# Kernel optimization log

Hardware: AMD Instinct MI355X
Metric: run time of the kernel (lower is better)

Reference implementation:

```python
import jax, jax.numpy as jnp
import numpy as np

EPS = 1e-8


def setup_inputs() -> dict:
    key = jax.random.key(0)
    k1, k2, k3 = jax.random.split(key, 3)
    B, N, M, C = 4, 4096, 16384, 256
    xyz = jax.random.normal(k1, (B * N, 3), dtype=jnp.float32)
    new_xyz = jax.random.normal(k2, (B * M, 3), dtype=jnp.float32)
    feat = jax.random.normal(k3, (B * N, C), dtype=jnp.float32)
    offset = jnp.arange(1, B + 1, dtype=jnp.int64) * N      # [4096, 8192, 12288, 16384]
    new_offset = jnp.arange(1, B + 1, dtype=jnp.int64) * M  # [16384, ..., 65536]
    return {"xyz": xyz, "new_xyz": new_xyz, "feat": feat,
            "offset": offset, "new_offset": new_offset, "k": 3}


def _interpolate(xyz_b, new_xyz_b, feat_b, k):
    # xyz_b: [B,N,3], new_xyz_b: [B,M,3], feat_b: [B,N,C]
    # pairwise squared distances via GEMM: [B,M,N]
    q2 = jnp.sum(new_xyz_b * new_xyz_b, axis=-1, keepdims=True)        # [B,M,1]
    s2 = jnp.sum(xyz_b * xyz_b, axis=-1)[:, None, :]                   # [B,1,N]
    cross = jnp.einsum('bmd,bnd->bmn', new_xyz_b, xyz_b)               # [B,M,N]
    d2 = q2 + s2 - 2.0 * cross                                         # [B,M,N]
    neg_d2, idx = jax.lax.top_k(-d2, k)                                # [B,M,k]
    dist = jnp.sqrt(jnp.maximum(-neg_d2, 1e-12))                       # euclidean, like knnquery
    dist_recip = 1.0 / (dist + EPS)
    weight = dist_recip / jnp.sum(dist_recip, axis=-1, keepdims=True)  # [B,M,k]
    gathered = jax.vmap(lambda f, i: f[i])(feat_b, idx)                # [B,M,k,C]
    return jnp.einsum('bmkc,bmk->bmc', gathered, weight)               # [B,M,C]


def reference(xyz, new_xyz, feat, offset, new_offset, k):
    B = offset.shape[0]
    N = xyz.shape[0] // B
    M = new_xyz.shape[0] // B
    C = feat.shape[1]
    # uniform offsets -> reshape into per-cloud batches
    out = _interpolate(xyz.reshape(B, N, 3), new_xyz.reshape(B, M, 3),
                       feat.reshape(B, N, C), k)
    return out.reshape(B * M, C)
```

## Files before the change

kernel.cpp:

```cpp
#include <hip/hip_runtime.h>
#include <float.h>


#define QPL   2
#define QPB   128
#define SPLIT 8
#define KEY_INIT 0x7FEFFFFFFFFFFFFFULL

#define NCA   16
#define NC    (NCA * NCA * NCA)
#define GMIN  (-4.0f)
#define HCELL (0.5f)
#define INVH  (2.0f)
#define SLACK (1e-3f)

typedef float v2f __attribute__((ext_vector_type(2)));

__device__ __forceinline__ double mk_key(float d2, int j) {
    unsigned long long u =
        ((unsigned long long)(unsigned)__float_as_uint(d2) << 32) | (unsigned)j;
    return __longlong_as_double(u);
}

__device__ __forceinline__ void ins3(double key, double& k0, double& k1,
                                     double& k2) {
    const double n0 = fmin(key, k0);
    const double n1 = fmin(fmax(key, k0), k1);
    const double n2 = fmin(fmax(key, k1), k2);
    k0 = n0; k1 = n1; k2 = n2;
}

__device__ __forceinline__ v2f dist2_pair(const v2f qx2, const v2f qy2,
                                          const v2f qz2, const v2f q22,
                                          const float4 p) {
    #pragma clang fp contract(off)
    const v2f px = {p.x, p.x};
    const v2f py = {p.y, p.y};
    const v2f pz = {p.z, p.z};
    const v2f pw = {p.w, p.w};
    const v2f t0 = qx2 * px;
    const v2f t1 = qy2 * py;
    const v2f t2 = t0 + t1;
    const v2f t3 = qz2 * pz;
    const v2f cr = t2 + t3;
    const v2f qs = q22 + pw;
    const v2f cc = cr + cr;
    const v2f d2 = qs - cc;
    return d2;
}

__device__ __forceinline__ float dist2_scalar(float qx, float qy, float qz,
                                              float q2, const float4 p) {
    #pragma clang fp contract(off)
    const float t0 = qx * p.x;
    const float t1 = qy * p.y;
    const float t2 = t0 + t1;
    const float t3 = qz * p.z;
    const float cr = t2 + t3;
    const float qs = q2 + p.w;
    const float cc = cr + cr;
    const float d2 = qs - cc;
    return d2;
}

__device__ __forceinline__ float sum_sq3(float x, float y, float z) {
    return __fadd_rn(__fadd_rn(__fmul_rn(x, x), __fmul_rn(y, y)),
                     __fmul_rn(z, z));
}

__device__ __forceinline__ int clampi(int v, int lo, int hi) {
    return v < lo ? lo : (v > hi ? hi : v);
}

__device__ __forceinline__ void cell3(float x, float y, float z,
                                      int& cx, int& cy, int& cz) {
    cx = clampi((int)floorf((x - GMIN) * INVH), 0, NCA - 1);
    cy = clampi((int)floorf((y - GMIN) * INVH), 0, NCA - 1);
    cz = clampi((int)floorf((z - GMIN) * INVH), 0, NCA - 1);
}

__global__ void grid_histo(const float* __restrict__ xyz,
                           const float* __restrict__ new_xyz,
                           int* __restrict__ cnt, int* __restrict__ qcnt,
                           int N, int M, int B) {
    const int i = blockIdx.x * blockDim.x + threadIdx.x;
    const int totalP = B * N;
    if (i < totalP) {
        const int b = i / N;
        int cx, cy, cz;
        cell3(xyz[(size_t)i * 3 + 0], xyz[(size_t)i * 3 + 1],
              xyz[(size_t)i * 3 + 2], cx, cy, cz);
        atomicAdd(&cnt[b * NC + (cz * NCA + cy) * NCA + cx], 1);
    } else {
        const int qi = i - totalP;
        if (qi < B * M) {
            const int b = qi / M;
            int cx, cy, cz;
            cell3(new_xyz[(size_t)qi * 3 + 0], new_xyz[(size_t)qi * 3 + 1],
                  new_xyz[(size_t)qi * 3 + 2], cx, cy, cz);
            atomicAdd(&qcnt[b * NC + (cz * NCA + cy) * NCA + cx], 1);
        }
    }
}

__global__ __launch_bounds__(256) void grid_scan(
    const int* __restrict__ cnt, int* __restrict__ start,
    const int* __restrict__ qcnt, int* __restrict__ qstart,
    int N, int M, int B) {
    const int blk = blockIdx.x;
    const bool isQ = blk >= B;
    const int b = isQ ? blk - B : blk;
    const int* __restrict__ src = isQ ? qcnt : cnt;
    int* __restrict__ dst = isQ ? qstart : start;
    const int base = isQ ? b * M : b * N;
    const int t = threadIdx.x;
    const int CH = NC / 256;

    int s = 0;
    for (int j = 0; j < CH; ++j) s += src[b * NC + t * CH + j];

    __shared__ int parts[256];
    parts[t] = s;
    __syncthreads();
    for (int off = 1; off < 256; off <<= 1) {
        int v = 0;
        if (t >= off) v = parts[t - off];
        __syncthreads();
        parts[t] += v;
        __syncthreads();
    }
    int run = base + (t == 0 ? 0 : parts[t - 1]);
    for (int j = 0; j < CH; ++j) {
        dst[b * NC + t * CH + j] = run;
        run += src[b * NC + t * CH + j];
    }
    if (!isQ && b == B - 1 && t == 255) dst[B * NC] = B * N;
}

__global__ void grid_scatter(const float* __restrict__ xyz,
                             const float* __restrict__ new_xyz,
                             int* __restrict__ cnt, int* __restrict__ qcnt,
                             const int* __restrict__ start,
                             const int* __restrict__ qstart,
                             float4* __restrict__ spts, int* __restrict__ sidx,
                             int* __restrict__ qsrt,
                             int N, int M, int B) {
    const int i = blockIdx.x * blockDim.x + threadIdx.x;
    const int totalP = B * N;
    if (i < totalP) {
        const int b = i / N;
        const float sx = xyz[(size_t)i * 3 + 0];
        const float sy = xyz[(size_t)i * 3 + 1];
        const float sz = xyz[(size_t)i * 3 + 2];
        int cx, cy, cz;
        cell3(sx, sy, sz, cx, cy, cz);
        const int g = b * NC + (cz * NCA + cy) * NCA + cx;
        const int slot = start[g] + (atomicSub(&cnt[g], 1) - 1);
        spts[slot] = make_float4(sx, sy, sz, sum_sq3(sx, sy, sz));
        sidx[slot] = i - b * N;
    } else {
        const int qi = i - totalP;
        if (qi < B * M) {
            const int b = qi / M;
            int cx, cy, cz;
            cell3(new_xyz[(size_t)qi * 3 + 0], new_xyz[(size_t)qi * 3 + 1],
                  new_xyz[(size_t)qi * 3 + 2], cx, cy, cz);
            const int g = b * NC + (cz * NCA + cy) * NCA + cx;
            const int slot = qstart[g] + (atomicSub(&qcnt[g], 1) - 1);
            qsrt[slot] = qi;
        }
    }
}

__global__ __launch_bounds__(256, 8) void fp_knn_gather(
    const float* __restrict__ new_xyz,
    const float4* __restrict__ spts, const int* __restrict__ sidx,
    const int* __restrict__ start, const int* __restrict__ qsrt,
    const float4* __restrict__ feat4, float4* __restrict__ out4,
    int N, int M, int B) {
    __shared__ int   s_jb[16][3];
    __shared__ float s_wb[16][3];
    __shared__ int   s_qid[16];

    const int tid = threadIdx.x;
    const int grp = tid >> 4;
    const int s   = tid & 15;
    const int p   = blockIdx.x * 16 + grp;
    const int qid = qsrt[p];
    const int b   = qid / M;
    const int bNC = b * NC;

    const float qx = new_xyz[(size_t)qid * 3 + 0];
    const float qy = new_xyz[(size_t)qid * 3 + 1];
    const float qz = new_xyz[(size_t)qid * 3 + 2];
    const float q2 = sum_sq3(qx, qy, qz);

    int cx, cy, cz;
    cell3(qx, qy, qz, cx, cy, cz);

    const float bx0 = GMIN + (float)cx * HCELL;
    const float by0 = GMIN + (float)cy * HCELL;
    const float bz0 = GMIN + (float)cz * HCELL;
    const float ex = fmaxf(fmaxf(bx0 - qx, qx - (bx0 + HCELL)), 0.0f);
    const float ey = fmaxf(fmaxf(by0 - qy, qy - (by0 + HCELL)), 0.0f);
    const float ez = fmaxf(fmaxf(bz0 - qz, qz - (bz0 + HCELL)), 0.0f);
    const float e = fmaxf(ex, fmaxf(ey, ez));

    double k0 = __longlong_as_double(KEY_INIT), k1 = k0, k2 = k0;

    auto seg = [&](int x0, int x1, int cy2, int cz2) {
        const int rowbase = bNC + (cz2 * NCA + cy2) * NCA;
        const int j0 = start[rowbase + x0];
        const int j1 = start[rowbase + x1 + 1];
        for (int j = j0 + s; j < j1; j += 16) {
            const float4 pt = spts[j];
            const float d2 = dist2_scalar(qx, qy, qz, q2, pt);
            ins3(mk_key(d2, sidx[j]), k0, k1, k2);
        }
    };

    auto merge16 = [&](double& o0, double& o1, double& o2) {
        double t0 = k0, t1 = k1, t2 = k2;
        #pragma unroll
        for (int mask = 1; mask <= 8; mask <<= 1) {
            const double r0 = __shfl_xor(t0, mask, 16);
            const double r1 = __shfl_xor(t1, mask, 16);
            const double r2 = __shfl_xor(t2, mask, 16);
            ins3(r0, t0, t1, t2);
            ins3(r1, t0, t1, t2);
            ins3(r2, t0, t1, t2);
        }
        o0 = t0; o1 = t1; o2 = t2;
    };

    {
        const int z0 = clampi(cz - 1, 0, NCA - 1), z1 = clampi(cz + 1, 0, NCA - 1);
        const int y0 = clampi(cy - 1, 0, NCA - 1), y1 = clampi(cy + 1, 0, NCA - 1);
        const int x0 = clampi(cx - 1, 0, NCA - 1), x1 = clampi(cx + 1, 0, NCA - 1);
        for (int cz2 = z0; cz2 <= z1; ++cz2)
            for (int cy2 = y0; cy2 <= y1; ++cy2)
                seg(x0, x1, cy2, cz2);
    }

    for (int r = 2; r < NCA; ++r) {
        double m0, m1, m2;
        merge16(m0, m1, m2);
        const float d3 = __uint_as_float(
            (unsigned)((unsigned long long)__double_as_longlong(m2) >> 32));
        const float lb = fmaxf(HCELL * (float)(r - 1) - e, 0.0f);
        if (lb * lb > d3 + SLACK) break;
        const int z0 = clampi(cz - r, 0, NCA - 1), z1 = clampi(cz + r, 0, NCA - 1);
        const int y0 = clampi(cy - r, 0, NCA - 1), y1 = clampi(cy + r, 0, NCA - 1);
        const int x0 = clampi(cx - r, 0, NCA - 1), x1 = clampi(cx + r, 0, NCA - 1);
        for (int cz2 = z0; cz2 <= z1; ++cz2) {
            const int adz = cz2 >= cz ? cz2 - cz : cz - cz2;
            for (int cy2 = y0; cy2 <= y1; ++cy2) {
                const int ady = cy2 >= cy ? cy2 - cy : cy - cy2;
                if (adz == r || ady == r) {
                    seg(x0, x1, cy2, cz2);
                } else {
                    if (cx - r >= 0)       seg(cx - r, cx - r, cy2, cz2);
                    if (cx + r <= NCA - 1) seg(cx + r, cx + r, cy2, cz2);
                }
            }
        }
    }

    double f0, f1, f2;
    merge16(f0, f1, f2);
    if (s == 0) {
        const unsigned long long u0 = __double_as_longlong(f0);
        const unsigned long long u1 = __double_as_longlong(f1);
        const unsigned long long u2 = __double_as_longlong(f2);
        const float d0 = __uint_as_float((unsigned)(u0 >> 32));
        const float d1 = __uint_as_float((unsigned)(u1 >> 32));
        const float d2f = __uint_as_float((unsigned)(u2 >> 32));
        const float e0 = sqrtf(fmaxf(d0, 1e-12f));
        const float e1 = sqrtf(fmaxf(d1, 1e-12f));
        const float e2 = sqrtf(fmaxf(d2f, 1e-12f));
        const float r0 = 1.0f / (e0 + 1e-8f);
        const float r1 = 1.0f / (e1 + 1e-8f);
        const float r2 = 1.0f / (e2 + 1e-8f);
        const float rs = r0 + r1 + r2;
        s_jb[grp][0] = (int)(u0 & 0xffffffffu);
        s_jb[grp][1] = (int)(u1 & 0xffffffffu);
        s_jb[grp][2] = (int)(u2 & 0xffffffffu);
        s_wb[grp][0] = r0 / rs; s_wb[grp][1] = r1 / rs; s_wb[grp][2] = r2 / rs;
        s_qid[grp] = qid;
    }
    __syncthreads();

    const int lane = tid & 63;
    const int wv   = tid >> 6;
    #pragma unroll
    for (int t = 0; t < 4; ++t) {
        const int qq = wv * 4 + t;
        const int qid2 = s_qid[qq];
        const int b2 = qid2 / M;
        const int src_base = b2 * N;
        const int   a0 = s_jb[qq][0], a1 = s_jb[qq][1], a2 = s_jb[qq][2];
        const float u0 = s_wb[qq][0], u1 = s_wb[qq][1], u2 = s_wb[qq][2];
        const float4 f0v = feat4[(size_t)(src_base + a0) * 64 + lane];
        const float4 f1v = feat4[(size_t)(src_base + a1) * 64 + lane];
        const float4 f2v = feat4[(size_t)(src_base + a2) * 64 + lane];
        float4 o;
        o.x = u0 * f0v.x + u1 * f1v.x + u2 * f2v.x;
        o.y = u0 * f0v.y + u1 * f1v.y + u2 * f2v.y;
        o.z = u0 * f0v.z + u1 * f1v.z + u2 * f2v.z;
        o.w = u0 * f0v.w + u1 * f1v.w + u2 * f2v.w;
        out4[(size_t)qid2 * 64 + lane] = o;
    }
}

__global__ void pack_pts(const float* __restrict__ xyz,
                         float4* __restrict__ pts, int total) {
    int i = blockIdx.x * blockDim.x + threadIdx.x;
    if (i < total) {
        const float sx = xyz[(size_t)i * 3 + 0];
        const float sy = xyz[(size_t)i * 3 + 1];
        const float sz = xyz[(size_t)i * 3 + 2];
        pts[i] = make_float4(sx, sy, sz, sum_sq3(sx, sy, sz));
    }
}

template <int CHUNK>
__global__ __launch_bounds__(512, 4) void fp_knn_main(
    const float* __restrict__ new_xyz, const float4* __restrict__ pts,
    const float4* __restrict__ feat4, float4* __restrict__ out4,
    int N, int blocks_per_batch) {
    __shared__ double s_k[SPLIT][QPB][3];
    __shared__ float  s_w[QPB][3];
    __shared__ int    s_j[QPB][3];

    int g = blockIdx.x;
    if (gridDim.x == 512 && blocks_per_batch == 128) {
        const int xcd = g & 7, slot = g >> 3;
        g = (xcd >> 1) * 128 + (xcd & 1) * 64 + slot;
    }

    const int tid  = threadIdx.x;
    const int lane = tid & 63;
    const int b    = g / blocks_per_batch;
    const int src_base = b * N;
    const int m0 = g * QPB + lane;
    const int m1 = m0 + 64;

    const float q0x = new_xyz[(size_t)m0 * 3 + 0];
    const float q0y = new_xyz[(size_t)m0 * 3 + 1];
    const float q0z = new_xyz[(size_t)m0 * 3 + 2];
    const float q1x = new_xyz[(size_t)m1 * 3 + 0];
    const float q1y = new_xyz[(size_t)m1 * 3 + 1];
    const float q1z = new_xyz[(size_t)m1 * 3 + 2];
    const v2f qx2 = {q0x, q1x};
    const v2f qy2 = {q0y, q1y};
    const v2f qz2 = {q0z, q1z};
    const v2f q22 = {sum_sq3(q0x, q0y, q0z), sum_sq3(q1x, q1y, q1z)};

    const int cw    = tid >> 6;
    const int cbase = cw * CHUNK;
    const float4* __restrict__ cp = pts + src_base + cbase;

    double k00 = __longlong_as_double(KEY_INIT);
    double k01 = k00, k02 = k00;
    double k10 = k00, k11 = k00, k12 = k00;

    #pragma unroll 8
    for (int j = 0; j < CHUNK; ++j) {
        const float4 p = cp[j];
        const v2f d2 = dist2_pair(qx2, qy2, qz2, q22, p);
        ins3(mk_key(d2.x, cbase + j), k00, k01, k02);
        ins3(mk_key(d2.y, cbase + j), k10, k11, k12);
    }

    s_k[cw][lane][0]      = k00; s_k[cw][lane][1]      = k01; s_k[cw][lane][2]      = k02;
    s_k[cw][lane + 64][0] = k10; s_k[cw][lane + 64][1] = k11; s_k[cw][lane + 64][2] = k12;
    __syncthreads();

    if (tid < QPB) {
        double m0k = __longlong_as_double(KEY_INIT), m1k = m0k, m2k = m0k;
        #pragma unroll
        for (int ss = 0; ss < SPLIT; ++ss) {
            #pragma unroll
            for (int r = 0; r < 3; ++r) ins3(s_k[ss][tid][r], m0k, m1k, m2k);
        }
        unsigned long long u0 = __double_as_longlong(m0k);
        unsigned long long u1 = __double_as_longlong(m1k);
        unsigned long long u2 = __double_as_longlong(m2k);
        const float d0 = __uint_as_float((unsigned)(u0 >> 32));
        const float d1 = __uint_as_float((unsigned)(u1 >> 32));
        const float d2 = __uint_as_float((unsigned)(u2 >> 32));
        const float e0 = sqrtf(fmaxf(d0, 1e-12f));
        const float e1 = sqrtf(fmaxf(d1, 1e-12f));
        const float e2 = sqrtf(fmaxf(d2, 1e-12f));
        const float r0 = 1.0f / (e0 + 1e-8f);
        const float r1 = 1.0f / (e1 + 1e-8f);
        const float r2 = 1.0f / (e2 + 1e-8f);
        const float rs = r0 + r1 + r2;
        s_w[tid][0] = r0 / rs; s_w[tid][1] = r1 / rs; s_w[tid][2] = r2 / rs;
        s_j[tid][0] = (int)(u0 & 0xffffffffu);
        s_j[tid][1] = (int)(u1 & 0xffffffffu);
        s_j[tid][2] = (int)(u2 & 0xffffffffu);
    }
    __syncthreads();

    const int wv    = tid >> 6;
    const int qbase = g * QPB;
    #pragma unroll 4
    for (int t = 0; t < QPB / SPLIT; ++t) {
        const int qq = wv * (QPB / SPLIT) + t;
        const int   a0 = s_j[qq][0], a1 = s_j[qq][1], a2 = s_j[qq][2];
        const float u0 = s_w[qq][0], u1 = s_w[qq][1], u2 = s_w[qq][2];
        const float4 f0 = feat4[(size_t)(src_base + a0) * 64 + lane];
        const float4 f1 = feat4[(size_t)(src_base + a1) * 64 + lane];
        const float4 f2 = feat4[(size_t)(src_base + a2) * 64 + lane];
        float4 o;
        o.x = u0 * f0.x + u1 * f1.x + u2 * f2.x;
        o.y = u0 * f0.y + u1 * f1.y + u2 * f2.y;
        o.z = u0 * f0.z + u1 * f1.z + u2 * f2.z;
        o.w = u0 * f0.w + u1 * f1.w + u2 * f2.w;
        out4[(size_t)(qbase + qq) * 64 + lane] = o;
    }
}

__global__ void fp_knn_generic(
    const float* __restrict__ new_xyz, const float* __restrict__ xyz,
    const float* __restrict__ feat, float* __restrict__ out,
    int N, int M, int Btot) {
    const int m = blockIdx.x * blockDim.x + threadIdx.x;
    if (m >= Btot * M) return;
    const int b = m / M;
    const int src_base = b * N;
    const float qx = new_xyz[(size_t)m * 3 + 0];
    const float qy = new_xyz[(size_t)m * 3 + 1];
    const float qz = new_xyz[(size_t)m * 3 + 2];
    const float q2 = sum_sq3(qx, qy, qz);
    double k0 = __longlong_as_double(KEY_INIT), k1 = k0, k2 = k0;
    for (int j = 0; j < N; ++j) {
        const float sx = xyz[(size_t)(src_base + j) * 3 + 0];
        const float sy = xyz[(size_t)(src_base + j) * 3 + 1];
        const float sz = xyz[(size_t)(src_base + j) * 3 + 2];
        const float4 p = make_float4(sx, sy, sz, sum_sq3(sx, sy, sz));
        const float d2 = dist2_scalar(qx, qy, qz, q2, p);
        ins3(mk_key(d2, j), k0, k1, k2);
    }
    unsigned long long u0 = __double_as_longlong(k0);
    unsigned long long u1 = __double_as_longlong(k1);
    unsigned long long u2 = __double_as_longlong(k2);
    const float e0 = sqrtf(fmaxf(__uint_as_float((unsigned)(u0 >> 32)), 1e-12f));
    const float e1 = sqrtf(fmaxf(__uint_as_float((unsigned)(u1 >> 32)), 1e-12f));
    const float e2 = sqrtf(fmaxf(__uint_as_float((unsigned)(u2 >> 32)), 1e-12f));
    const float r0 = 1.0f / (e0 + 1e-8f);
    const float r1 = 1.0f / (e1 + 1e-8f);
    const float r2 = 1.0f / (e2 + 1e-8f);
    const float rs = r0 + r1 + r2;
    const float w0 = r0 / rs, w1 = r1 / rs, w2 = r2 / rs;
    const int a0 = (int)(u0 & 0xffffffffu), a1 = (int)(u1 & 0xffffffffu),
              a2 = (int)(u2 & 0xffffffffu);
    const int C = 256;
    for (int c = 0; c < C; ++c) {
        out[(size_t)m * C + c] =
            w0 * feat[(size_t)(src_base + a0) * C + c] +
            w1 * feat[(size_t)(src_base + a1) * C + c] +
            w2 * feat[(size_t)(src_base + a2) * C + c];
    }
}

extern "C" void kernel_launch(void* const* d_in, const int* in_sizes, int n_in,
                              void* d_out, int out_size, void* d_ws, size_t ws_size,
                              hipStream_t stream) {
    const float* xyz     = (const float*)d_in[0];
    const float* new_xyz = (const float*)d_in[1];
    const float* feat    = (const float*)d_in[2];
    float* out = (float*)d_out;

    const int B = in_sizes[3];
    const int N = in_sizes[0] / (3 * B);
    const int M = in_sizes[1] / (3 * B);
    const int Q = B * M;

    auto al = [](size_t x) { return (x + 255) & ~(size_t)255; };
    const size_t o_spts   = 0;
    const size_t o_sidx   = o_spts  + al((size_t)B * N * 16);
    const size_t o_cnt    = o_sidx  + al((size_t)B * N * 4);
    const size_t o_qcnt   = o_cnt   + al((size_t)B * NC * 4);
    const size_t o_start  = o_qcnt  + al((size_t)B * NC * 4);
    const size_t o_qstart = o_start + al(((size_t)B * NC + 1) * 4);
    const size_t o_qsort  = o_qstart+ al(((size_t)B * NC + 1) * 4);
    const size_t need_grid = o_qsort + al((size_t)Q * 4);

    if ((Q % 16 == 0) && ws_size >= need_grid) {
        char* w = (char*)d_ws;
        float4* spts  = (float4*)(w + o_spts);
        int*   sidx   = (int*)  (w + o_sidx);
        int*   cnt    = (int*)  (w + o_cnt);
        int*   qcnt   = (int*)  (w + o_qcnt);
        int*   start  = (int*)  (w + o_start);
        int*   qstart = (int*)  (w + o_qstart);
        int*   qsrt   = (int*)  (w + o_qsort);

        hipMemsetAsync(cnt, 0, o_start - o_cnt, stream);
        const int items = B * N + B * M;
        grid_histo<<<(items + 255) / 256, 256, 0, stream>>>(
            xyz, new_xyz, cnt, qcnt, N, M, B);
        grid_scan<<<2 * B, 256, 0, stream>>>(cnt, start, qcnt, qstart, N, M, B);
        grid_scatter<<<(items + 255) / 256, 256, 0, stream>>>(
            xyz, new_xyz, cnt, qcnt, start, qstart, spts, sidx, qsrt, N, M, B);
        fp_knn_gather<<<Q / 16, 256, 0, stream>>>(
            new_xyz, spts, sidx, start, qsrt, (const float4*)feat,
            (float4*)out, N, M, B);
        return;
    }

    const size_t pts_bytes = (size_t)(B * N) * sizeof(float4);
    const bool fused_ok = (N % SPLIT == 0) && (N / SPLIT == 512) &&
                          (M % QPB == 0) && (ws_size >= pts_bytes);
    if (fused_ok) {
        pack_pts<<<(B * N + 255) / 256, 256, 0, stream>>>(xyz, (float4*)d_ws, B * N);
        const int blocks = Q / QPB;
        fp_knn_main<512><<<blocks, 512, 0, stream>>>(
            new_xyz, (const float4*)d_ws, (const float4*)feat, (float4*)out,
            N, M / QPB);
    } else {
        fp_knn_generic<<<(Q + 255) / 256, 256, 0, stream>>>(
            new_xyz, xyz, feat, out, N, M, B);
    }
}
```

Measured before the change: 199.5 us.

## Fuse grid histogram, scan and scatter into one per-cloud LDS kernel

Replaces the memset plus three grid-building kernels (global-atomic histogram, scan, scatter) with a single kernel that runs one 1024-thread block per cloud, for points and for queries. Each block builds its cell histogram in shared memory, scans it, and scatters with shared atomics. This removes three launches, the memset and the global atomic traffic. In exchange only 2*B blocks do this work, so parallelism is low for large clouds, and the scatter order within a cell becomes nondeterministic.

```diff
diff --git a/kernel.cpp b/kernel.cpp
--- a/kernel.cpp
+++ b/kernel.cpp
@@ -79,95 +79,69 @@
     cz = clampi((int)floorf((z - GMIN) * INVH), 0, NCA - 1);
 }
 
-__global__ void grid_histo(const float* __restrict__ xyz,
-                           const float* __restrict__ new_xyz,
-                           int* __restrict__ cnt, int* __restrict__ qcnt,
-                           int N, int M, int B) {
-    const int i = blockIdx.x * blockDim.x + threadIdx.x;
-    const int totalP = B * N;
-    if (i < totalP) {
-        const int b = i / N;
-        int cx, cy, cz;
-        cell3(xyz[(size_t)i * 3 + 0], xyz[(size_t)i * 3 + 1],
-              xyz[(size_t)i * 3 + 2], cx, cy, cz);
-        atomicAdd(&cnt[b * NC + (cz * NCA + cy) * NCA + cx], 1);
-    } else {
-        const int qi = i - totalP;
-        if (qi < B * M) {
-            const int b = qi / M;
-            int cx, cy, cz;
-            cell3(new_xyz[(size_t)qi * 3 + 0], new_xyz[(size_t)qi * 3 + 1],
-                  new_xyz[(size_t)qi * 3 + 2], cx, cy, cz);
-            atomicAdd(&qcnt[b * NC + (cz * NCA + cy) * NCA + cx], 1);
-        }
-    }
-}
-
-__global__ __launch_bounds__(256) void grid_scan(
-    const int* __restrict__ cnt, int* __restrict__ start,
-    const int* __restrict__ qcnt, int* __restrict__ qstart,
-    int N, int M, int B) {
+__global__ __launch_bounds__(1024) void grid_build(
+    const float* __restrict__ xyz, const float* __restrict__ new_xyz,
+    int* __restrict__ start, int* __restrict__ qstart,
+    float4* __restrict__ spts, int* __restrict__ sidx,
+    int* __restrict__ qsrt, int N, int M, int B)
+{
+    __shared__ int hist[NC];
+    __shared__ int psum[1024];
+
     const int blk = blockIdx.x;
     const bool isQ = blk >= B;
     const int b = isQ ? blk - B : blk;
-    const int* __restrict__ src = isQ ? qcnt : cnt;
+    const int nItems = isQ ? M : N;
+    const float* __restrict__ src = isQ ? new_xyz + (size_t)b * M * 3
+                                        : xyz + (size_t)b * N * 3;
     int* __restrict__ dst = isQ ? qstart : start;
     const int base = isQ ? b * M : b * N;
     const int t = threadIdx.x;
-    const int CH = NC / 256;
-
-    int s = 0;
-    for (int j = 0; j < CH; ++j) s += src[b * NC + t * CH + j];
-
-    __shared__ int parts[256];
-    parts[t] = s;
-    __syncthreads();
-    for (int off = 1; off < 256; off <<= 1) {
+
+    #pragma unroll
+    for (int c = t; c < NC; c += 1024) hist[c] = 0;
+    __syncthreads();
+
+    for (int i = t; i < nItems; i += 1024) {
+        int cx, cy, cz;
+        cell3(src[(size_t)i * 3 + 0], src[(size_t)i * 3 + 1],
+              src[(size_t)i * 3 + 2], cx, cy, cz);
+        atomicAdd(&hist[(cz * NCA + cy) * NCA + cx], 1);
+    }
+    __syncthreads();
+
+    int loc0 = hist[t * 4 + 0], loc1 = hist[t * 4 + 1];
+    int loc2 = hist[t * 4 + 2], loc3 = hist[t * 4 + 3];
+    psum[t] = loc0 + loc1 + loc2 + loc3;
+    __syncthreads();
+    for (int off = 1; off < 1024; off <<= 1) {
         int v = 0;
-        if (t >= off) v = parts[t - off];
+        if (t >= off) v = psum[t - off];
         __syncthreads();
-        parts[t] += v;
+        psum[t] += v;
         __syncthreads();
     }
-    int run = base + (t == 0 ? 0 : parts[t - 1]);
-    for (int j = 0; j < CH; ++j) {
-        dst[b * NC + t * CH + j] = run;
-        run += src[b * NC + t * CH + j];
-    }
-    if (!isQ && b == B - 1 && t == 255) dst[B * NC] = B * N;
-}
-
-__global__ void grid_scatter(const float* __restrict__ xyz,
-                             const float* __restrict__ new_xyz,
-                             int* __restrict__ cnt, int* __restrict__ qcnt,
-                             const int* __restrict__ start,
-                             const int* __restrict__ qstart,
-                             float4* __restrict__ spts, int* __restrict__ sidx,
-                             int* __restrict__ qsrt,
-                             int N, int M, int B) {
-    const int i = blockIdx.x * blockDim.x + threadIdx.x;
-    const int totalP = B * N;
-    if (i < totalP) {
-        const int b = i / N;
-        const float sx = xyz[(size_t)i * 3 + 0];
-        const float sy = xyz[(size_t)i * 3 + 1];
-        const float sz = xyz[(size_t)i * 3 + 2];
+    int run = (t == 0 ? 0 : psum[t - 1]);
+    dst[b * NC + t * 4 + 0] = base + run;  hist[t * 4 + 0] = run;  run += loc0;
+    dst[b * NC + t * 4 + 1] = base + run;  hist[t * 4 + 1] = run;  run += loc1;
+    dst[b * NC + t * 4 + 2] = base + run;  hist[t * 4 + 2] = run;  run += loc2;
+    dst[b * NC + t * 4 + 3] = base + run;  hist[t * 4 + 3] = run;  run += loc3;
+    if (!isQ && b == B - 1 && t == 1023) start[B * NC] = B * N;
+    __syncthreads();
+
+    for (int i = t; i < nItems; i += 1024) {
+        const float x = src[(size_t)i * 3 + 0];
+        const float y = src[(size_t)i * 3 + 1];
+        const float z = src[(size_t)i * 3 + 2];
         int cx, cy, cz;
-        cell3(sx, sy, sz, cx, cy, cz);
-        const int g = b * NC + (cz * NCA + cy) * NCA + cx;
-        const int slot = start[g] + (atomicSub(&cnt[g], 1) - 1);
-        spts[slot] = make_float4(sx, sy, sz, sum_sq3(sx, sy, sz));
-        sidx[slot] = i - b * N;
-    } else {
-        const int qi = i - totalP;
-        if (qi < B * M) {
-            const int b = qi / M;
-            int cx, cy, cz;
-            cell3(new_xyz[(size_t)qi * 3 + 0], new_xyz[(size_t)qi * 3 + 1],
-                  new_xyz[(size_t)qi * 3 + 2], cx, cy, cz);
-            const int g = b * NC + (cz * NCA + cy) * NCA + cx;
-            const int slot = qstart[g] + (atomicSub(&qcnt[g], 1) - 1);
-            qsrt[slot] = qi;
+        cell3(x, y, z, cx, cy, cz);
+        const int c = (cz * NCA + cy) * NCA + cx;
+        const int slot = base + atomicAdd(&hist[c], 1);
+        if (isQ) {
+            qsrt[slot] = b * M + i;
+        } else {
+            spts[slot] = make_float4(x, y, z, sum_sq3(x, y, z));
+            sidx[slot] = i;
         }
     }
 }
@@ -481,30 +455,21 @@
     auto al = [](size_t x) { return (x + 255) & ~(size_t)255; };
     const size_t o_spts   = 0;
     const size_t o_sidx   = o_spts  + al((size_t)B * N * 16);
-    const size_t o_cnt    = o_sidx  + al((size_t)B * N * 4);
-    const size_t o_qcnt   = o_cnt   + al((size_t)B * NC * 4);
-    const size_t o_start  = o_qcnt  + al((size_t)B * NC * 4);
+    const size_t o_start  = o_sidx  + al((size_t)B * N * 4);
     const size_t o_qstart = o_start + al(((size_t)B * NC + 1) * 4);
-    const size_t o_qsort  = o_qstart+ al(((size_t)B * NC + 1) * 4);
+    const size_t o_qsort  = o_qstart+ al((size_t)B * NC * 4);
     const size_t need_grid = o_qsort + al((size_t)Q * 4);
 
     if ((Q % 16 == 0) && ws_size >= need_grid) {
         char* w = (char*)d_ws;
         float4* spts  = (float4*)(w + o_spts);
         int*   sidx   = (int*)  (w + o_sidx);
-        int*   cnt    = (int*)  (w + o_cnt);
-        int*   qcnt   = (int*)  (w + o_qcnt);
         int*   start  = (int*)  (w + o_start);
         int*   qstart = (int*)  (w + o_qstart);
         int*   qsrt   = (int*)  (w + o_qsort);
 
-        hipMemsetAsync(cnt, 0, o_start - o_cnt, stream);
-        const int items = B * N + B * M;
-        grid_histo<<<(items + 255) / 256, 256, 0, stream>>>(
-            xyz, new_xyz, cnt, qcnt, N, M, B);
-        grid_scan<<<2 * B, 256, 0, stream>>>(cnt, start, qcnt, qstart, N, M, B);
-        grid_scatter<<<(items + 255) / 256, 256, 0, stream>>>(
-            xyz, new_xyz, cnt, qcnt, start, qstart, spts, sidx, qsrt, N, M, B);
+        grid_build<<<2 * B, 1024, 0, stream>>>(
+            xyz, new_xyz, start, qstart, spts, sidx, qsrt, N, M, B);
         fp_knn_gather<<<Q / 16, 256, 0, stream>>>(
             new_xyz, spts, sidx, start, qsrt, (const float4*)feat,
             (float4*)out, N, M, B);
```

Result: no change. 199.7 us (median of 2 runs) (+0.1%).
